# Kernel optimization log

Hardware: AMD Instinct MI355X
Metric: run time of the kernel (lower is better)

The kernel has to match this reference:

```python
import jax, jax.numpy as jnp
import numpy as np

N, E, H, NH, S, EF, K = 25000, 400000, 64, 4, 16, 8, 2
HS = H // NH  # head size


def _ln(x, w, b):
    m = x.mean(-1, keepdims=True)
    v = ((x - m) ** 2).mean(-1, keepdims=True)
    return (x - m) / jnp.sqrt(v + 1e-5) * w + b


def _seg_softmax(scores, seg, n):
    # scores: [E, NH], seg: [E] -> softmax over edges sharing the same dest node
    mx = jax.ops.segment_max(scores, seg, num_segments=n)
    e = jnp.exp(scores - mx[seg])
    s = jax.ops.segment_sum(e, seg, num_segments=n)
    return e / (s[seg] + 1e-9)


def _edge_layer(h, x_s, src, dest, ef, w1, w2, proj, gated):
    # h: [N,H] (already layer-normed). Gather, fused per-edge MLP (no bias).
    inp = jnp.concatenate([h[src], h[dest], x_s[src], x_s[dest], ef], axis=-1)  # [E,168]
    raw = jnp.maximum(inp @ w1.T, 0.0) @ w2.T  # [E,NH]
    if gated:
        w = jax.nn.sigmoid(raw)
    else:
        w = _seg_softmax(jax.nn.leaky_relu(raw) / jnp.sqrt(jnp.asarray(HS, raw.dtype)), dest, N)
    msg = h.reshape(N, NH, HS)[src] * w[:, :, None]          # [E,NH,HS]
    agg = jax.ops.segment_sum(msg, dest, num_segments=N)     # [N,NH,HS]
    return agg.reshape(N, H) @ proj.T, w


def _mlp(x, w1, b1, w2, b2):
    return jnp.maximum(x @ w1.T + b1, 0.0) @ w2.T + b2


def _forward(x, x_s, edge_features, fwd_w1, fwd_w2, fwd_proj, rev_w1, rev_w2, rev_proj,
             ln_w, ln_b, r_w1, r_b1, r_w2, r_b2, z_w1, z_b1, z_w2, z_b2,
             c_w1, c_b1, c_w2, c_b2, edge_index):
    src, dest = edge_index[0], edge_index[1]
    # forward-direction stacked attention hops
    h_fwd, fwd_ws = x, []
    for k in range(K):
        h_norm = _ln(h_fwd, ln_w, ln_b)
        msg, w = _edge_layer(h_norm, x_s, src, dest, edge_features,
                             fwd_w1[k], fwd_w2[k], fwd_proj[k], gated=False)
        h_fwd = h_fwd + msg
        fwd_ws.append(w)
    fwd_ws = jnp.stack(fwd_ws, axis=-1)  # [E,NH,K]
    # reverse-direction stacked gating hops (edge direction flipped)
    h_rev, rev_ws = x, []
    for k in range(K):
        h_norm = _ln(h_rev, ln_w, ln_b)
        msg, w = _edge_layer(h_norm, x_s, dest, src, edge_features,
                             rev_w1[k], rev_w2[k], rev_proj[k], gated=True)
        h_rev = h_rev + msg
        rev_ws.append(w)
    rev_ws = jnp.stack(rev_ws, axis=-1)  # [E,NH,K]
    messages = jnp.concatenate([h_fwd - x, h_rev - x], axis=-1)  # [N,2H]
    gate_input = jnp.concatenate([x, messages], axis=-1)          # [N,3H]
    r_gate = jax.nn.sigmoid(_mlp(gate_input, r_w1, r_b1, r_w2, r_b2))
    z_gate = jax.nn.sigmoid(_mlp(gate_input, z_w1, z_b1, z_w2, z_b2))
    cand_in = jnp.concatenate([r_gate * x, messages], axis=-1)
    cand = jnp.tanh(_mlp(cand_in, c_w1, c_b1, c_w2, c_b2))
    final_h = (1.0 - z_gate) * x + z_gate * cand
    return final_h, fwd_ws, rev_ws, z_gate, r_gate


def setup_inputs() -> dict:
    key = jax.random.key(0)
    ks = jax.random.split(key, 20)
    mlp_in = 2 * H + 2 * S + EF  # 168
    width = 2 * H                # 128
    gi, gw = 3 * H, 3 * H        # 192, 192

    def nrm(k, shape, fan_in):
        return jax.random.normal(k, shape, jnp.float32) / np.sqrt(fan_in)

    return {
        'x': jax.random.normal(ks[0], (N, H), jnp.float32),
        'x_s': jax.random.normal(ks[1], (N, S), jnp.float32),
        'edge_index': jax.random.randint(ks[2], (2, E), 0, N, jnp.int32),
        'edge_features': jax.random.normal(ks[3], (E, EF), jnp.float32),
        'fwd_w1': nrm(ks[4], (K, width, mlp_in), mlp_in),
        'fwd_w2': nrm(ks[5], (K, NH, width), width),
        'fwd_proj': nrm(ks[6], (K, H, H), H),
        'rev_w1': nrm(ks[7], (K, width, mlp_in), mlp_in),
        'rev_w2': nrm(ks[8], (K, NH, width), width),
        'rev_proj': nrm(ks[9], (K, H, H), H),
        'ln_w': jnp.ones((H,), jnp.float32),
        'ln_b': jnp.zeros((H,), jnp.float32),
        'r_w1': nrm(ks[10], (gw, gi), gi), 'r_b1': jnp.zeros((gw,), jnp.float32),
        'r_w2': nrm(ks[11], (H, gw), gw), 'r_b2': jnp.zeros((H,), jnp.float32),
        'z_w1': nrm(ks[12], (gw, gi), gi), 'z_b1': jnp.zeros((gw,), jnp.float32),
        'z_w2': nrm(ks[13], (H, gw), gw), 'z_b2': jnp.zeros((H,), jnp.float32),
        'c_w1': nrm(ks[14], (gw, gi), gi), 'c_b1': jnp.zeros((gw,), jnp.float32),
        'c_w2': nrm(ks[15], (H, gw), gw), 'c_b2': jnp.zeros((H,), jnp.float32),
    }


def reference(x, x_s, edge_index, edge_features, fwd_w1, fwd_w2, fwd_proj,
              rev_w1, rev_w2, rev_proj, ln_w, ln_b, r_w1, r_b1, r_w2, r_b2,
              z_w1, z_b1, z_w2, z_b2, c_w1, c_b1, c_w2, c_b2):
    return _forward(x, x_s, edge_features, fwd_w1, fwd_w2, fwd_proj,
                    rev_w1, rev_w2, rev_proj, ln_w, ln_b,
                    r_w1, r_b1, r_w2, r_b2, z_w1, z_b1, z_w2, z_b2,
                    c_w1, c_b1, c_w2, c_b2, edge_index)
```

## Files before the change

### kernel.cpp

```cpp
#include <hip/hip_runtime.h>
#include <math.h>

#define NN 25000
#define EE 400000
#define HH 64
#define NHEAD 4
#define SDIM 16
#define EFDIM 8
#define KHOP 2
#define MIN 168
#define WID 128
#define GIN 192
#define KP 96

typedef __attribute__((ext_vector_type(8))) short bf16x8;
typedef __attribute__((ext_vector_type(4))) float f32x4;
typedef unsigned short ushortT;
typedef unsigned int uintT;

__device__ __forceinline__ float wave_sum64(float v) {
#pragma unroll
  for (int m = 1; m <= 32; m <<= 1) v += __shfl_xor(v, m, 64);
  return v;
}

__device__ __forceinline__ ushortT f2b(float f) {
  uintT u = __float_as_uint(f);
  return (ushortT)((u + 0x7FFFu + ((u >> 16) & 1u)) >> 16);
}
__device__ __forceinline__ float b2f(ushortT h) {
  return __uint_as_float(((uintT)h) << 16);
}
__device__ __forceinline__ float b2f_lo(uintT u) { return __uint_as_float(u << 16); }
__device__ __forceinline__ float b2f_hi(uintT u) { return __uint_as_float(u & 0xffff0000u); }

__global__ void k_histo2(const int* __restrict__ src, const int* __restrict__ dst,
                         int* __restrict__ cnt_s, int* __restrict__ cnt_d) {
  int e = blockIdx.x * 256 + threadIdx.x;
  if (e < EE) {
    atomicAdd(&cnt_d[dst[e]], 1);
    atomicAdd(&cnt_s[src[e]], 1);
  }
}

__global__ void k_scan2(const int* __restrict__ cnt_d, const int* __restrict__ cnt_s,
                        int* __restrict__ rp_d, int* __restrict__ rp_s) {
  const int* cnt = blockIdx.x ? cnt_s : cnt_d;
  int* rp = blockIdx.x ? rp_s : rp_d;
  __shared__ int part[1024];
  int t = threadIdx.x;
  const int CH = (NN + 1023) / 1024;
  int base = t * CH;
  int s = 0;
  for (int i = 0; i < CH; ++i) {
    int j = base + i;
    if (j < NN) s += cnt[j];
  }
  part[t] = s;
  __syncthreads();
  for (int off = 1; off < 1024; off <<= 1) {
    int v = (t >= off) ? part[t - off] : 0;
    __syncthreads();
    part[t] += v;
    __syncthreads();
  }
  int run = (t == 0) ? 0 : part[t - 1];
  for (int i = 0; i < CH; ++i) {
    int j = base + i;
    if (j < NN) { rp[j] = run; run += cnt[j]; }
  }
  if (t == 1023) rp[NN] = run;
}

__global__ void k_scatter2(const int* __restrict__ src, const int* __restrict__ dst,
                           const int* __restrict__ rp_s, const int* __restrict__ rp_d,
                           int* __restrict__ cur_s, int* __restrict__ cur_d,
                           int* __restrict__ eid_s, int* __restrict__ eid_d) {
  int e = blockIdx.x * 256 + threadIdx.x;
  if (e < EE) {
    int nd = dst[e];
    int pd = atomicAdd(&cur_d[nd], 1);
    eid_d[rp_d[nd] + pd] = e;
    int ns = src[e];
    int ps = atomicAdd(&cur_s[ns], 1);
    eid_s[rp_s[ns] + ps] = e;
  }
}

__global__ __launch_bounds__(256) void k_sortseg2(const int* __restrict__ rp_d,
                                                  const int* __restrict__ rp_s,
                                                  int* __restrict__ eid_d,
                                                  int* __restrict__ eid_s) {
  int gw = blockIdx.x * 4 + (threadIdx.x >> 6);
  int lane = threadIdx.x & 63;
  if (gw >= 2 * NN) return;
  const int* rp = (gw < NN) ? rp_d : rp_s;
  int* eids = (gw < NN) ? eid_d : eid_s;
  int node = (gw < NN) ? gw : gw - NN;
  int beg = rp[node], end = rp[node + 1];
  int deg = end - beg;
  if (deg <= 1) return;
  if (deg <= 64) {
    int v = (lane < deg) ? eids[beg + lane] : 0x7fffffff;
#pragma unroll
    for (int k = 2; k <= 64; k <<= 1) {
#pragma unroll
      for (int j = k >> 1; j > 0; j >>= 1) {
        int other = __shfl_xor(v, j, 64);
        bool takeMin = (((lane & k) == 0) == ((lane & j) == 0));
        v = takeMin ? min(v, other) : max(v, other);
      }
    }
    if (lane < deg) eids[beg + lane] = v;
  } else if (lane == 0) {
    for (int i = beg + 1; i < end; ++i) {
      int v = eids[i];
      int j = i - 1;
      while (j >= beg && eids[j] > v) { eids[j + 1] = eids[j]; --j; }
      eids[j + 1] = v;
    }
  }
}

__global__ void k_mkpos2(const int* __restrict__ eid_d, const int* __restrict__ eid_s,
                         const int* __restrict__ src, const int* __restrict__ dst,
                         const float* __restrict__ ef, int4* __restrict__ pos_f,
                         int4* __restrict__ pos_r, float4* __restrict__ efs_f,
                         float4* __restrict__ efs_r) {
  int i = blockIdx.x * 256 + threadIdx.x;
  if (i >= EE) return;
  int e1 = eid_d[i];
  pos_f[i] = make_int4(e1, src[e1], dst[e1], 0);
  int e2 = eid_s[i];
  pos_r[i] = make_int4(e2, dst[e2], src[e2], 0);
  efs_f[2 * i] = *(const float4*)(ef + (size_t)e1 * EFDIM);
  efs_f[2 * i + 1] = *(const float4*)(ef + (size_t)e1 * EFDIM + 4);
  efs_r[2 * i] = *(const float4*)(ef + (size_t)e2 * EFDIM);
  efs_r[2 * i + 1] = *(const float4*)(ef + (size_t)e2 * EFDIM + 4);
}

#define PACKN (256 * KP + 8 * 128)
__global__ void k_pack_bf(const float* __restrict__ fw1, const float* __restrict__ rw1,
                          ushortT* __restrict__ pAB_all, float* __restrict__ pE_all) {
  int y = blockIdx.y;
  const float* w1 = (y < 2) ? fw1 + (size_t)y * WID * MIN
                            : rw1 + (size_t)(y - 2) * WID * MIN;
  ushortT* pAB = pAB_all + (size_t)y * 256 * KP;
  float* pE = pE_all + (size_t)y * 8 * 128;
  int i = blockIdx.x * 256 + threadIdx.x;
  if (i < 256 * KP) {
    int j = i / KP, k = i % KP;
    float v = 0.f;
    if (k < 80) {
      int row = (j < 128) ? j : j - 128;
      int col = (j < 128) ? (k < 64 ? k : k + 64) : (k < 64 ? k + 64 : k + 80);
      v = w1[row * MIN + col];
    }
    pAB[i] = f2b(v);
  } else if (i < PACKN) {
    int ii = i - 256 * KP;
    int f = ii >> 7, j = ii & 127;
    pE[ii] = w1[j * MIN + 160 + f];
  }
}

#define CW1 (GIN * GIN)
#define CW2 (HH * GIN)
__global__ void k_cvt6(const float* __restrict__ r_w1, const float* __restrict__ z_w1,
                       const float* __restrict__ c_w1, const float* __restrict__ r_w2,
                       const float* __restrict__ z_w2, const float* __restrict__ c_w2,
                       ushortT* __restrict__ rzw1, ushortT* __restrict__ cw1,
                       ushortT* __restrict__ rw2, ushortT* __restrict__ zw2,
                       ushortT* __restrict__ cw2) {
  int i = blockIdx.x * 256 + threadIdx.x;
  if (i < CW1) rzw1[i] = f2b(r_w1[i]);
  else if (i < 2 * CW1) rzw1[i] = f2b(z_w1[i - CW1]);
  else if (i < 3 * CW1) cw1[i - 2 * CW1] = f2b(c_w1[i - 2 * CW1]);
  else if (i < 3 * CW1 + CW2) rw2[i - 3 * CW1] = f2b(r_w2[i - 3 * CW1]);
  else if (i < 3 * CW1 + 2 * CW2) zw2[i - 3 * CW1 - CW2] = f2b(z_w2[i - 3 * CW1 - CW2]);
  else if (i < 3 * CW1 + 3 * CW2) cw2[i - 3 * CW1 - 2 * CW2] = f2b(c_w2[i - 3 * CW1 - 2 * CW2]);
}

__global__ __launch_bounds__(256) void k_ln2(const float* __restrict__ hf,
                                             const float* __restrict__ hr,
                                             const float* __restrict__ xs,
                                             const float* __restrict__ lw,
                                             const float* __restrict__ lb,
                                             ushortT* __restrict__ ncf,
                                             ushortT* __restrict__ ncr) {
  const float* h = blockIdx.y ? hr : hf;
  ushortT* nodecat = blockIdx.y ? ncr : ncf;
  int t = threadIdx.x;
  int node = blockIdx.x * 4 + (t >> 6), lane = t & 63;
  if (node >= NN) return;
  float v = h[(size_t)node * HH + lane];
  float mean = wave_sum64(v) * (1.0f / 64.0f);
  float d = v - mean;
  float var = wave_sum64(d * d) * (1.0f / 64.0f);
  nodecat[(size_t)node * KP + lane] = f2b(d * rsqrtf(var + 1e-5f) * lw[lane] + lb[lane]);
  if (lane < SDIM) {
    nodecat[(size_t)node * KP + HH + lane] = f2b(xs[(size_t)node * SDIM + lane]);
    nodecat[(size_t)node * KP + 80 + lane] = 0;
  }
}

__global__ __launch_bounds__(256) void k_proj2(
    const ushortT* __restrict__ Af, const ushortT* __restrict__ Ar,
    const ushortT* __restrict__ Wf, const ushortT* __restrict__ Wr,
    ushortT* __restrict__ Cf, ushortT* __restrict__ Cr) {
  const ushortT* A = blockIdx.y ? Ar : Af;
  const ushortT* W = blockIdx.y ? Wr : Wf;
  ushortT* C = blockIdx.y ? Cr : Cf;
  int w = threadIdx.x >> 6, l = threadIdx.x & 63;
  int m0 = blockIdx.x * 64 + w * 16;
  int rowa = m0 + (l & 15);
  int kb = l >> 4;
  bf16x8 afr0 = {0,0,0,0,0,0,0,0}, afr1 = afr0, afr2 = afr0;
  if (rowa < NN) {
    const ushortT* ap = A + (size_t)rowa * KP + kb * 8;
    afr0 = *(const bf16x8*)(ap);
    afr1 = *(const bf16x8*)(ap + 32);
    afr2 = *(const bf16x8*)(ap + 64);
  }
  int crow = m0 + (l >> 4) * 4;
  int ccol0 = l & 15;
  for (int n0 = 0; n0 < 256; n0 += 64) {
    f32x4 acc[4];
#pragma unroll
    for (int n = 0; n < 4; ++n) acc[n] = (f32x4){0.f, 0.f, 0.f, 0.f};
    const ushortT* wbase = W + (size_t)(n0 + (l & 15)) * KP + kb * 8;
#pragma unroll
    for (int n = 0; n < 4; ++n) {
      const ushortT* wp = wbase + (size_t)(16 * n) * KP;
      acc[n] = __builtin_amdgcn_mfma_f32_16x16x32_bf16(afr0, *(const bf16x8*)(wp), acc[n], 0, 0, 0);
      acc[n] = __builtin_amdgcn_mfma_f32_16x16x32_bf16(afr1, *(const bf16x8*)(wp + 32), acc[n], 0, 0, 0);
      acc[n] = __builtin_amdgcn_mfma_f32_16x16x32_bf16(afr2, *(const bf16x8*)(wp + 64), acc[n], 0, 0, 0);
    }
#pragma unroll
    for (int n = 0; n < 4; ++n) {
      int col = n0 + ccol0 + n * 16;
#pragma unroll
      for (int r = 0; r < 4; ++r) {
        int row = crow + r;
        if (row < NN) C[(size_t)row * 256 + col] = f2b(acc[n][r]);
      }
    }
  }
}

template <int ACT, int BF16OUT, int KD>
__global__ __launch_bounds__(256) void k_gemm2(
    const ushortT* __restrict__ A, int lda, const ushortT* __restrict__ W,
    const float* __restrict__ bias, void* __restrict__ Cout, int ldc, int M, int Nc,
    const float* __restrict__ zv, const float* __restrict__ xp) {
  constexpr int KS = KD / 32;
  int w = threadIdx.x >> 6, l = threadIdx.x & 63;
  int m0 = blockIdx.x * 64 + w * 16;
  int rowa = m0 + (l & 15);
  int kb = l >> 4;
  bf16x8 afr[KS];
#pragma unroll
  for (int ks = 0; ks < KS; ++ks) {
    afr[ks] = (bf16x8){0, 0, 0, 0, 0, 0, 0, 0};
    if (rowa < M) afr[ks] = *(const bf16x8*)(A + (size_t)rowa * lda + ks * 32 + kb * 8);
  }
  int crow = m0 + (l >> 4) * 4;
  int ccol0 = l & 15;
  for (int n0 = 0; n0 < Nc; n0 += 64) {
    f32x4 acc[4];
#pragma unroll
    for (int n = 0; n < 4; ++n) acc[n] = (f32x4){0.f, 0.f, 0.f, 0.f};
    const ushortT* wbase = W + (size_t)(n0 + (l & 15)) * KD + kb * 8;
#pragma unroll
    for (int n = 0; n < 4; ++n) {
      const ushortT* wp = wbase + (size_t)(16 * n) * KD;
#pragma unroll
      for (int ks = 0; ks < KS; ++ks)
        acc[n] = __builtin_amdgcn_mfma_f32_16x16x32_bf16(afr[ks], *(const bf16x8*)(wp + ks * 32),
                                                         acc[n], 0, 0, 0);
    }
#pragma unroll
    for (int n = 0; n < 4; ++n) {
      int col = n0 + ccol0 + n * 16;
      float bv = bias ? bias[col] : 0.f;
#pragma unroll
      for (int r = 0; r < 4; ++r) {
        int row = crow + r;
        if (row < M) {
          float v = acc[n][r] + bv;
          if (ACT == 1) v = fmaxf(v, 0.f);
          else if (ACT == 2) v = 1.f / (1.f + expf(-v));
          else if (ACT == 3) v = tanhf(v);
          else if (ACT == 5) {
            float z = zv[(size_t)row * HH + col];
            float xv = xp[(size_t)row * HH + col];
            v = (1.f - z) * xv + z * tanhf(v);
          }
          if (BF16OUT)
            ((ushortT*)Cout)[(size_t)row * ldc + col] = f2b(v);
          else
            ((float*)Cout)[(size_t)row * ldc + col] = v;
        }
      }
    }
  }
}

__global__ __launch_bounds__(256) void k_gemm_rz(
    const ushortT* __restrict__ hid, const ushortT* __restrict__ rw2,
    const ushortT* __restrict__ zw2, const float* __restrict__ rb2,
    const float* __restrict__ zb2, float* __restrict__ outR, float* __restrict__ outZ) {
  int y = blockIdx.y;
  const ushortT* A = hid + (y ? GIN : 0);
  const ushortT* W = y ? zw2 : rw2;
  const float* bias = y ? zb2 : rb2;
  float* C = y ? outZ : outR;
  constexpr int KS = GIN / 32;
  int w = threadIdx.x >> 6, l = threadIdx.x & 63;
  int m0 = blockIdx.x * 64 + w * 16;
  int rowa = m0 + (l & 15);
  int kb = l >> 4;
  bf16x8 afr[KS];
#pragma unroll
  for (int ks = 0; ks < KS; ++ks) {
    afr[ks] = (bf16x8){0, 0, 0, 0, 0, 0, 0, 0};
    if (rowa < NN) afr[ks] = *(const bf16x8*)(A + (size_t)rowa * 384 + ks * 32 + kb * 8);
  }
  int crow = m0 + (l >> 4) * 4;
  int ccol0 = l & 15;
  f32x4 acc[4];
#pragma unroll
  for (int n = 0; n < 4; ++n) acc[n] = (f32x4){0.f, 0.f, 0.f, 0.f};
  const ushortT* wbase = W + (size_t)(l & 15) * GIN + kb * 8;
#pragma unroll
  for (int n = 0; n < 4; ++n) {
    const ushortT* wp = wbase + (size_t)(16 * n) * GIN;
#pragma unroll
    for (int ks = 0; ks < KS; ++ks)
      acc[n] = __builtin_amdgcn_mfma_f32_16x16x32_bf16(afr[ks], *(const bf16x8*)(wp + ks * 32),
                                                       acc[n], 0, 0, 0);
  }
#pragma unroll
  for (int n = 0; n < 4; ++n) {
    int col = ccol0 + n * 16;
    float bv = bias[col];
#pragma unroll
    for (int r = 0; r < 4; ++r) {
      int row = crow + r;
      if (row < NN) {
        float v = acc[n][r] + bv;
        C[(size_t)row * HH + col] = 1.f / (1.f + expf(-v));
      }
    }
  }
}

__global__ __launch_bounds__(256) void k_edge3(
    const ushortT* __restrict__ cABf, const ushortT* __restrict__ cABr,
    const int4* __restrict__ pos_f, const int4* __restrict__ pos_r,
    const float4* __restrict__ efs_f, const float4* __restrict__ efs_r,
    const float* __restrict__ w1e_f, const float* __restrict__ w1e_r,
    const float* __restrict__ w2f, const float* __restrict__ w2r,
    float* __restrict__ s_seq, float* __restrict__ outRW,
    float* __restrict__ ws_seq, int hop) {
  int y = blockIdx.y;
  const ushortT* cAB = y ? cABr : cABf;
  const int4* pos = y ? pos_r : pos_f;
  const float4* efs = y ? efs_r : efs_f;
  const float* w1e = y ? w1e_r : w1e_f;
  const float* w2 = y ? w2r : w2f;
  __shared__ float w1e_s[8][128];
  __shared__ float w2_s[4][128];
  int t = threadIdx.x;
  for (int i = t; i < 1024; i += 256) w1e_s[i >> 7][i & 127] = w1e[i];
  for (int i = t; i < 512; i += 256) w2_s[i >> 7][i & 127] = w2[i];
  __syncthreads();
  int es = t >> 2, q = t & 3;
  size_t ii = (size_t)blockIdx.x * 64 + es;
  int4 pr = pos[ii];
  const ushortT* cA = cAB + (size_t)pr.y * 256;
  const ushortT* cBp = cAB + (size_t)pr.z * 256 + 128;
  float4 e0 = efs[2 * ii], e1 = efs[2 * ii + 1];
  float efv[8] = {e0.x, e0.y, e0.z, e0.w, e1.x, e1.y, e1.z, e1.w};
  float p[4] = {0.f, 0.f, 0.f, 0.f};
#pragma unroll
  for (int c = 0; c < 4; ++c) {
    int j = c * 32 + q * 8;
    uint4 ua4 = *(const uint4*)(cA + j);
    uint4 ub4 = *(const uint4*)(cBp + j);
    const uintT* au = (const uintT*)&ua4;
    const uintT* bu = (const uintT*)&ub4;
    float h[8];
#pragma unroll
    for (int i2 = 0; i2 < 4; ++i2) {
      h[2 * i2] = b2f_lo(au[i2]) + b2f_lo(bu[i2]);
      h[2 * i2 + 1] = b2f_hi(au[i2]) + b2f_hi(bu[i2]);
    }
#pragma unroll
    for (int f = 0; f < 8; ++f) {
      float ev = efv[f];
      float4 w0 = *(const float4*)(&w1e_s[f][j]);
      float4 w1v = *(const float4*)(&w1e_s[f][j + 4]);
      h[0] += ev * w0.x; h[1] += ev * w0.y; h[2] += ev * w0.z; h[3] += ev * w0.w;
      h[4] += ev * w1v.x; h[5] += ev * w1v.y; h[6] += ev * w1v.z; h[7] += ev * w1v.w;
    }
#pragma unroll
    for (int i2 = 0; i2 < 8; ++i2) h[i2] = fmaxf(h[i2], 0.f);
#pragma unroll
    for (int o = 0; o < 4; ++o) {
      float4 u0 = *(const float4*)(&w2_s[o][j]);
      float4 u1 = *(const float4*)(&w2_s[o][j + 4]);
      p[o] += h[0] * u0.x + h[1] * u0.y + h[2] * u0.z + h[3] * u0.w +
              h[4] * u1.x + h[5] * u1.y + h[6] * u1.z + h[7] * u1.w;
    }
  }
#pragma unroll
  for (int o = 0; o < 4; ++o) {
    p[o] += __shfl_xor(p[o], 1, 64);
    p[o] += __shfl_xor(p[o], 2, 64);
  }
  float pv = (q == 0) ? p[0] : (q == 1) ? p[1] : (q == 2) ? p[2] : p[3];
  if (y) {
    float sig = 1.f / (1.f + expf(-pv));
    outRW[(size_t)pr.x * (NHEAD * KHOP) + q * KHOP + hop] = sig;
    ws_seq[ii * 4 + q] = sig;
  } else {
    s_seq[ii * 4 + q] = (pv > 0.f ? pv : 0.01f * pv) * 0.25f;
  }
}

template <int SM>
__global__ __launch_bounds__(256) void k_softagg(
    const ushortT* __restrict__ hn_bf, const float* __restrict__ s_seq,
    const float* __restrict__ ws_seq, int hop, const int* __restrict__ rp,
    const int4* __restrict__ pos, const float* __restrict__ proj,
    float* __restrict__ h, float* __restrict__ wout) {
  __shared__ float proj_s[64][68];
  __shared__ float agg_s[4][64];
  __shared__ float w_s[4][64][4];
  int t = threadIdx.x;
  for (int i = t; i < 4096; i += 256) proj_s[i >> 6][i & 63] = proj[i];
  int wvi = t >> 6, lane = t & 63;
  int node = blockIdx.x * 4 + wvi;
  __syncthreads();

  float acc = 0.f;
  if (node < NN) {
    int beg = rp[node], end = rp[node + 1];
    int deg = end - beg;
    float mxv = 0.f, invv = 0.f;
    if (SM && deg > 0) {
      int li = lane >> 2, o = lane & 3;
      if (deg <= 64) {
        int i0 = beg + li;
        int ee4[4];
        float sv[4];
#pragma unroll
        for (int u = 0; u < 4; ++u) {
          int idx = i0 + u * 16;
          bool val = idx < end;
          int id2 = val ? idx : beg;
          ee4[u] = pos[id2].x;
          float v = s_seq[(size_t)id2 * 4 + o];
          sv[u] = val ? v : -1e30f;
        }
        float mx = fmaxf(fmaxf(sv[0], sv[1]), fmaxf(sv[2], sv[3]));
#pragma unroll
        for (int m = 4; m <= 32; m <<= 1) mx = fmaxf(mx, __shfl_xor(mx, m, 64));
        float ex[4];
        float sum = 0.f;
#pragma unroll
        for (int u = 0; u < 4; ++u) {
          ex[u] = (sv[u] > -1e29f) ? expf(sv[u] - mx) : 0.f;
          sum += ex[u];
        }
#pragma unroll
        for (int m = 4; m <= 32; m <<= 1) sum += __shfl_xor(sum, m, 64);
        float inv = 1.f / (sum + 1e-9f);
#pragma unroll
        for (int u = 0; u < 4; ++u) {
          if (i0 + u * 16 < end) {
            float wv = ex[u] * inv;
            wout[(size_t)ee4[u] * (NHEAD * KHOP) + o * KHOP + hop] = wv;
            w_s[wvi][li + u * 16][o] = wv;
          }
        }
      } else {
        float mx = -1e30f;
        for (int ii = beg + li; ii < end; ii += 16)
          mx = fmaxf(mx, s_seq[(size_t)ii * 4 + o]);
#pragma unroll
        for (int m = 4; m <= 32; m <<= 1) mx = fmaxf(mx, __shfl_xor(mx, m, 64));
        float sum = 0.f;
        for (int ii = beg + li; ii < end; ii += 16)
          sum += expf(s_seq[(size_t)ii * 4 + o] - mx);
#pragma unroll
        for (int m = 4; m <= 32; m <<= 1) sum += __shfl_xor(sum, m, 64);
        float inv = 1.f / (sum + 1e-9f);
        for (int ii = beg + li; ii < end; ii += 16) {
          wout[(size_t)pos[ii].x * (NHEAD * KHOP) + o * KHOP + hop] =
              expf(s_seq[(size_t)ii * 4 + o] - mx) * inv;
        }
        mxv = mx;
        invv = inv;
      }
    }
    int hd = lane >> 4;
    float mx_hd = 0.f, inv_hd = 0.f;
    if (SM) {
      mx_hd = __shfl(mxv, hd, 64);
      inv_hd = __shfl(invv, hd, 64);
    }
    bool useLds = (deg <= 64);
    for (int ii = beg; ii < end; ii += 8) {
      int idxv[8];
      int other[8];
      float wv8[8];
      float hv[8];
#pragma unroll
      for (int u = 0; u < 8; ++u) {
        int idx = ii + u;
        idxv[u] = (idx < end) ? idx : beg;
      }
#pragma unroll
      for (int u = 0; u < 8; ++u) other[u] = pos[idxv[u]].y;
#pragma unroll
      for (int u = 0; u < 8; ++u) {
        if (SM) {
          if (useLds)
            wv8[u] = w_s[wvi][idxv[u] - beg][hd];
          else
            wv8[u] = expf(s_seq[(size_t)idxv[u] * 4 + hd] - mx_hd) * inv_hd;
        } else {
          wv8[u] = ws_seq[(size_t)idxv[u] * 4 + hd];
        }
      }
#pragma unroll
      for (int u = 0; u < 8; ++u)
        hv[u] = b2f(hn_bf[(size_t)other[u] * KP + lane]);
#pragma unroll
      for (int u = 0; u < 8; ++u) {
        float w = (ii + u < end) ? wv8[u] : 0.f;
        acc += w * hv[u];
      }
    }
  }
  agg_s[wvi][lane] = acc;
  __syncthreads();
  if (node < NN) {
    float m = 0.f;
#pragma unroll
    for (int hh = 0; hh < 64; hh += 4) {
      float4 p = *(const float4*)(&proj_s[lane][hh]);
      m += p.x * agg_s[wvi][hh] + p.y * agg_s[wvi][hh + 1] +
           p.z * agg_s[wvi][hh + 2] + p.w * agg_s[wvi][hh + 3];
    }
    h[(size_t)node * HH + lane] += m;
  }
}

__global__ void k_gatein(const float* __restrict__ x, const float* __restrict__ hf,
                         const float* __restrict__ hr, ushortT* __restrict__ gi) {
  int g = blockIdx.x * 256 + threadIdx.x;
  if (g >= NN * HH) return;
  int node = g >> 6, j = g & 63;
  float xv = x[g];
  gi[(size_t)node * GIN + j] = f2b(xv);
  gi[(size_t)node * GIN + 64 + j] = f2b(hf[g] - xv);
  gi[(size_t)node * GIN + 128 + j] = f2b(hr[g] - xv);
}

__global__ void k_candin(const float* __restrict__ x, const float* __restrict__ r,
                         ushortT* __restrict__ gi) {
  int g = blockIdx.x * 256 + threadIdx.x;
  if (g >= NN * HH) return;
  gi[(size_t)(g >> 6) * GIN + (g & 63)] = f2b(r[g] * x[g]);
}

extern "C" void kernel_launch(void* const* d_in, const int* in_sizes, int n_in,
                              void* d_out, int out_size, void* d_ws, size_t ws_size,
                              hipStream_t stream) {
  const float* x = (const float*)d_in[0];
  const float* xs = (const float*)d_in[1];
  const int* ei = (const int*)d_in[2];
  const float* ef = (const float*)d_in[3];
  const float* fw1 = (const float*)d_in[4];
  const float* fw2 = (const float*)d_in[5];
  const float* fpj = (const float*)d_in[6];
  const float* rw1 = (const float*)d_in[7];
  const float* rw2 = (const float*)d_in[8];
  const float* rpj = (const float*)d_in[9];
  const float* lnw = (const float*)d_in[10];
  const float* lnb = (const float*)d_in[11];
  const float* r_w1 = (const float*)d_in[12];
  const float* r_b1 = (const float*)d_in[13];
  const float* r_w2 = (const float*)d_in[14];
  const float* r_b2 = (const float*)d_in[15];
  const float* z_w1 = (const float*)d_in[16];
  const float* z_b1 = (const float*)d_in[17];
  const float* z_w2 = (const float*)d_in[18];
  const float* z_b2 = (const float*)d_in[19];
  const float* c_w1 = (const float*)d_in[20];
  const float* c_b1 = (const float*)d_in[21];
  const float* c_w2 = (const float*)d_in[22];
  const float* c_b2 = (const float*)d_in[23];
  const int* srcp = ei;
  const int* dstp = ei + EE;

  float* outF = (float*)d_out;
  float* outFW = outF + (size_t)NN * HH;
  float* outRW = outFW + (size_t)EE * NHEAD * KHOP;
  float* outZ = outRW + (size_t)EE * NHEAD * KHOP;
  float* outR = outZ + (size_t)NN * HH;

  char* Wb = (char*)d_ws;
  size_t off = 0;
  auto alloc = [&](size_t bytes) -> void* {
    void* p = Wb + off;
    off += (bytes + 255) & ~(size_t)255;
    return p;
  };
  float* h_fwd = (float*)alloc((size_t)NN * HH * 4);
  float* h_rev = (float*)alloc((size_t)NN * HH * 4);
  ushortT* ncat_f = (ushortT*)alloc((size_t)NN * KP * 2);
  ushortT* ncat_r = (ushortT*)alloc((size_t)NN * KP * 2);
  float* s_seq = (float*)alloc((size_t)EE * NHEAD * 4);
  float* ws_seq = (float*)alloc((size_t)EE * NHEAD * 4);
  char* big = (char*)alloc((size_t)2 * NN * 256 * 2);
  ushortT* cAB_f = (ushortT*)big;
  ushortT* cAB_r = (ushortT*)(big + (size_t)NN * 256 * 2);
  ushortT* hid_bf = (ushortT*)big;
  ushortT* gi_bf = (ushortT*)alloc((size_t)NN * GIN * 2);
  ushortT* packAB_bf = (ushortT*)alloc((size_t)4 * 256 * KP * 2);
  float* packE = (float*)alloc((size_t)4 * 8 * 128 * 4);
  ushortT* rzw1_bf = (ushortT*)alloc((size_t)384 * GIN * 2);
  ushortT* rw2_bf = (ushortT*)alloc((size_t)HH * GIN * 2);
  ushortT* zw2_bf = (ushortT*)alloc((size_t)HH * GIN * 2);
  ushortT* cw1_bf = (ushortT*)alloc((size_t)GIN * GIN * 2);
  ushortT* cw2_bf = (ushortT*)alloc((size_t)HH * GIN * 2);
  float* rz_b1 = (float*)alloc(384 * 4);
  int* rp_d = (int*)alloc((NN + 8) * 4);
  int* rp_s = (int*)alloc((NN + 8) * 4);
  int* cur2 = (int*)alloc((size_t)2 * NN * 4);
  int* cur_d = cur2;
  int* cur_s = cur2 + NN;
  int* eid_d = (int*)alloc((size_t)EE * 4);
  int* eid_s = (int*)alloc((size_t)EE * 4);
  int4* pos_f = (int4*)alloc((size_t)EE * 16);
  int4* pos_r = (int4*)alloc((size_t)EE * 16);
  float4* efs_f = (float4*)alloc((size_t)EE * 32);
  float4* efs_r = (float4*)alloc((size_t)EE * 32);

  (void)hipMemcpyAsync(h_fwd, x, (size_t)NN * HH * 4, hipMemcpyDeviceToDevice, stream);
  (void)hipMemcpyAsync(h_rev, x, (size_t)NN * HH * 4, hipMemcpyDeviceToDevice, stream);
  (void)hipMemcpyAsync(rz_b1, r_b1, GIN * 4, hipMemcpyDeviceToDevice, stream);
  (void)hipMemcpyAsync(rz_b1 + GIN, z_b1, GIN * 4, hipMemcpyDeviceToDevice, stream);

  const int EB = (EE + 255) / 256, NW = (NN + 3) / 4;
  const int PB = (PACKN + 255) / 256;

  dim3 gPack(PB, 4);
  k_pack_bf<<<gPack, 256, 0, stream>>>(fw1, rw1, packAB_bf, packE);
  k_cvt6<<<(3 * CW1 + 3 * CW2 + 255) / 256, 256, 0, stream>>>(
      r_w1, z_w1, c_w1, r_w2, z_w2, c_w2, rzw1_bf, cw1_bf, rw2_bf, zw2_bf, cw2_bf);

  (void)hipMemsetAsync(cur2, 0, (size_t)2 * NN * 4, stream);
  k_histo2<<<EB, 256, 0, stream>>>(srcp, dstp, cur_s, cur_d);
  k_scan2<<<2, 1024, 0, stream>>>(cur_d, cur_s, rp_d, rp_s);
  (void)hipMemsetAsync(cur2, 0, (size_t)2 * NN * 4, stream);
  k_scatter2<<<EB, 256, 0, stream>>>(srcp, dstp, rp_s, rp_d, cur_s, cur_d, eid_s, eid_d);
  k_sortseg2<<<(2 * NN + 3) / 4, 256, 0, stream>>>(rp_d, rp_s, eid_d, eid_s);
  k_mkpos2<<<EB, 256, 0, stream>>>(eid_d, eid_s, srcp, dstp, ef, pos_f, pos_r, efs_f, efs_r);

  const int MB64 = (NN + 63) / 64;
  dim3 gLN(NW, 2), gProj(MB64, 2), gEdge(EE / 64, 2);
  for (int k = 0; k < KHOP; ++k) {
    k_ln2<<<gLN, 256, 0, stream>>>(h_fwd, h_rev, xs, lnw, lnb, ncat_f, ncat_r);
    k_proj2<<<gProj, 256, 0, stream>>>(ncat_f, ncat_r,
                                       packAB_bf + (size_t)k * 256 * KP,
                                       packAB_bf + (size_t)(2 + k) * 256 * KP,
                                       cAB_f, cAB_r);
    k_edge3<<<gEdge, 256, 0, stream>>>(cAB_f, cAB_r, pos_f, pos_r, efs_f, efs_r,
                                       packE + (size_t)k * 8 * 128,
                                       packE + (size_t)(2 + k) * 8 * 128,
                                       fw2 + (size_t)k * NHEAD * WID,
                                       rw2 + (size_t)k * NHEAD * WID,
                                       s_seq, outRW, ws_seq, k);
    k_softagg<1><<<NW, 256, 0, stream>>>(ncat_f, s_seq, nullptr, k, rp_d, pos_f,
                                         fpj + (size_t)k * HH * HH, h_fwd, outFW);
    k_softagg<0><<<NW, 256, 0, stream>>>(ncat_r, nullptr, ws_seq, k, rp_s, pos_r,
                                         rpj + (size_t)k * HH * HH, h_rev, nullptr);
  }

  k_gatein<<<(NN * HH) / 256, 256, 0, stream>>>(x, h_fwd, h_rev, gi_bf);
  k_gemm2<1, 1, GIN><<<MB64, 256, 0, stream>>>(gi_bf, GIN, rzw1_bf, rz_b1, hid_bf,
                                               384, NN, 384, nullptr, nullptr);
  dim3 gRZ(MB64, 2);
  k_gemm_rz<<<gRZ, 256, 0, stream>>>(hid_bf, rw2_bf, zw2_bf, r_b2, z_b2, outR, outZ);
  k_candin<<<(NN * HH) / 256, 256, 0, stream>>>(x, outR, gi_bf);
  k_gemm2<1, 1, GIN><<<MB64, 256, 0, stream>>>(gi_bf, GIN, cw1_bf, c_b1, hid_bf, GIN,
                                               NN, GIN, nullptr, nullptr);
  k_gemm2<5, 0, GIN><<<MB64, 256, 0, stream>>>(hid_bf, GIN, cw2_bf, c_b2, outF, HH,
                                               NN, HH, outZ, x);
}
```

Measured before the change: 609.5 us.

## Use fp16 packed math in edge MLP and fuse LN and gate prep into aggregation

The per-edge MLP now works in packed half2 arithmetic: the projected node features, edge features and second-layer weights are stored as fp16, halving gather bandwidth and doubling ALU throughput. LayerNorm for the next hop is fused into the aggregation kernel, and the forward and reverse aggregation launches are merged into one grid. Gate-input and candidate-input preparation are folded into the aggregation and r/z GEMM epilogues, removing separate kernels and extra passes over node arrays. The cost is reduced precision (fp16 range and accumulation inside the MLP) and more complex kernels.

```diff
diff --git a/kernel.cpp b/kernel.cpp
--- a/kernel.cpp
+++ b/kernel.cpp
@@ -1,4 +1,5 @@
 #include <hip/hip_runtime.h>
+#include <hip/hip_fp16.h>
 #include <math.h>
 
 #define NN 25000
@@ -31,8 +32,19 @@
 __device__ __forceinline__ float b2f(ushortT h) {
   return __uint_as_float(((uintT)h) << 16);
 }
-__device__ __forceinline__ float b2f_lo(uintT u) { return __uint_as_float(u << 16); }
-__device__ __forceinline__ float b2f_hi(uintT u) { return __uint_as_float(u & 0xffff0000u); }
+
+union U4H8 {
+  uint4 u;
+  __half2 h[4];
+};
+
+__device__ __forceinline__ __half2 relu2(__half2 v) {
+  union { __half2 h; uintT u; } x;
+  x.h = v;
+  uintT mask = ((x.u & 0x80008000u) >> 15) * 0xFFFFu;
+  x.u &= ~mask;
+  return x.h;
+}
 
 __global__ void k_histo2(const int* __restrict__ src, const int* __restrict__ dst,
                          int* __restrict__ cnt_s, int* __restrict__ cnt_d) {
@@ -125,28 +137,46 @@
 __global__ void k_mkpos2(const int* __restrict__ eid_d, const int* __restrict__ eid_s,
                          const int* __restrict__ src, const int* __restrict__ dst,
                          const float* __restrict__ ef, int4* __restrict__ pos_f,
-                         int4* __restrict__ pos_r, float4* __restrict__ efs_f,
-                         float4* __restrict__ efs_r) {
+                         int4* __restrict__ pos_r, uint4* __restrict__ efh_f,
+                         uint4* __restrict__ efh_r) {
   int i = blockIdx.x * 256 + threadIdx.x;
   if (i >= EE) return;
   int e1 = eid_d[i];
   pos_f[i] = make_int4(e1, src[e1], dst[e1], 0);
   int e2 = eid_s[i];
   pos_r[i] = make_int4(e2, dst[e2], src[e2], 0);
-  efs_f[2 * i] = *(const float4*)(ef + (size_t)e1 * EFDIM);
-  efs_f[2 * i + 1] = *(const float4*)(ef + (size_t)e1 * EFDIM + 4);
-  efs_r[2 * i] = *(const float4*)(ef + (size_t)e2 * EFDIM);
-  efs_r[2 * i + 1] = *(const float4*)(ef + (size_t)e2 * EFDIM + 4);
-}
-
-#define PACKN (256 * KP + 8 * 128)
+  {
+    float4 a0 = *(const float4*)(ef + (size_t)e1 * EFDIM);
+    float4 a1 = *(const float4*)(ef + (size_t)e1 * EFDIM + 4);
+    U4H8 u;
+    u.h[0] = __floats2half2_rn(a0.x, a0.y);
+    u.h[1] = __floats2half2_rn(a0.z, a0.w);
+    u.h[2] = __floats2half2_rn(a1.x, a1.y);
+    u.h[3] = __floats2half2_rn(a1.z, a1.w);
+    efh_f[i] = u.u;
+  }
+  {
+    float4 b0 = *(const float4*)(ef + (size_t)e2 * EFDIM);
+    float4 b1 = *(const float4*)(ef + (size_t)e2 * EFDIM + 4);
+    U4H8 u;
+    u.h[0] = __floats2half2_rn(b0.x, b0.y);
+    u.h[1] = __floats2half2_rn(b0.z, b0.w);
+    u.h[2] = __floats2half2_rn(b1.x, b1.y);
+    u.h[3] = __floats2half2_rn(b1.z, b1.w);
+    efh_r[i] = u.u;
+  }
+}
+
+#define PACKN (256 * KP + 512 + 256)
 __global__ void k_pack_bf(const float* __restrict__ fw1, const float* __restrict__ rw1,
-                          ushortT* __restrict__ pAB_all, float* __restrict__ pE_all) {
+                          const float* __restrict__ fw2, const float* __restrict__ rw2,
+                          ushortT* __restrict__ pAB_all, __half2* __restrict__ w1e2_all,
+                          __half2* __restrict__ w22_all) {
   int y = blockIdx.y;
   const float* w1 = (y < 2) ? fw1 + (size_t)y * WID * MIN
                             : rw1 + (size_t)(y - 2) * WID * MIN;
-  ushortT* pAB = pAB_all + (size_t)y * 256 * KP;
-  float* pE = pE_all + (size_t)y * 8 * 128;
+  const float* w2 = (y < 2) ? fw2 + (size_t)y * NHEAD * WID
+                            : rw2 + (size_t)(y - 2) * NHEAD * WID;
   int i = blockIdx.x * 256 + threadIdx.x;
   if (i < 256 * KP) {
     int j = i / KP, k = i % KP;
@@ -156,11 +186,16 @@
       int col = (j < 128) ? (k < 64 ? k : k + 64) : (k < 64 ? k + 64 : k + 80);
       v = w1[row * MIN + col];
     }
-    pAB[i] = f2b(v);
+    pAB_all[(size_t)y * 256 * KP + i] = f2b(v);
+  } else if (i < 256 * KP + 512) {
+    int jj = i - 256 * KP;
+    int f = jj >> 6, jp = jj & 63;
+    w1e2_all[y * 512 + jj] =
+        __floats2half2_rn(w1[(2 * jp) * MIN + 160 + f], w1[(2 * jp + 1) * MIN + 160 + f]);
   } else if (i < PACKN) {
-    int ii = i - 256 * KP;
-    int f = ii >> 7, j = ii & 127;
-    pE[ii] = w1[j * MIN + 160 + f];
+    int jj = i - 256 * KP - 512;
+    int o = jj >> 6, jp = jj & 63;
+    w22_all[y * 256 + jj] = __floats2half2_rn(w2[o * WID + 2 * jp], w2[o * WID + 2 * jp + 1]);
   }
 }
 
@@ -181,26 +216,31 @@
   else if (i < 3 * CW1 + 3 * CW2) cw2[i - 3 * CW1 - 2 * CW2] = f2b(c_w2[i - 3 * CW1 - 2 * CW2]);
 }
 
-__global__ __launch_bounds__(256) void k_ln2(const float* __restrict__ hf,
-                                             const float* __restrict__ hr,
-                                             const float* __restrict__ xs,
-                                             const float* __restrict__ lw,
-                                             const float* __restrict__ lb,
-                                             ushortT* __restrict__ ncf,
-                                             ushortT* __restrict__ ncr) {
-  const float* h = blockIdx.y ? hr : hf;
-  ushortT* nodecat = blockIdx.y ? ncr : ncf;
+__global__ __launch_bounds__(256) void k_ln_init(
+    const float* __restrict__ x, const float* __restrict__ xs,
+    const float* __restrict__ lw, const float* __restrict__ lb,
+    ushortT* __restrict__ ncf0, ushortT* __restrict__ ncr0,
+    ushortT* __restrict__ ncf1, ushortT* __restrict__ ncr1) {
   int t = threadIdx.x;
   int node = blockIdx.x * 4 + (t >> 6), lane = t & 63;
   if (node >= NN) return;
-  float v = h[(size_t)node * HH + lane];
+  float v = x[(size_t)node * HH + lane];
   float mean = wave_sum64(v) * (1.0f / 64.0f);
   float d = v - mean;
   float var = wave_sum64(d * d) * (1.0f / 64.0f);
-  nodecat[(size_t)node * KP + lane] = f2b(d * rsqrtf(var + 1e-5f) * lw[lane] + lb[lane]);
+  ushortT val = f2b(d * rsqrtf(var + 1e-5f) * lw[lane] + lb[lane]);
+  ncf0[(size_t)node * KP + lane] = val;
+  ncr0[(size_t)node * KP + lane] = val;
   if (lane < SDIM) {
-    nodecat[(size_t)node * KP + HH + lane] = f2b(xs[(size_t)node * SDIM + lane]);
-    nodecat[(size_t)node * KP + 80 + lane] = 0;
+    ushortT xv = f2b(xs[(size_t)node * SDIM + lane]);
+    ncf0[(size_t)node * KP + HH + lane] = xv;
+    ncr0[(size_t)node * KP + HH + lane] = xv;
+    ncf1[(size_t)node * KP + HH + lane] = xv;
+    ncr1[(size_t)node * KP + HH + lane] = xv;
+    ncf0[(size_t)node * KP + 80 + lane] = 0;
+    ncr0[(size_t)node * KP + 80 + lane] = 0;
+    ncf1[(size_t)node * KP + 80 + lane] = 0;
+    ncr1[(size_t)node * KP + 80 + lane] = 0;
   }
 }
 
@@ -242,7 +282,8 @@
 #pragma unroll
       for (int r = 0; r < 4; ++r) {
         int row = crow + r;
-        if (row < NN) C[(size_t)row * 256 + col] = f2b(acc[n][r]);
+        if (row < NN)
+          C[(size_t)row * 256 + col] = __half_as_ushort(__float2half(acc[n][r]));
       }
     }
   }
@@ -309,7 +350,8 @@
 __global__ __launch_bounds__(256) void k_gemm_rz(
     const ushortT* __restrict__ hid, const ushortT* __restrict__ rw2,
     const ushortT* __restrict__ zw2, const float* __restrict__ rb2,
-    const float* __restrict__ zb2, float* __restrict__ outR, float* __restrict__ outZ) {
+    const float* __restrict__ zb2, float* __restrict__ outR, float* __restrict__ outZ,
+    const float* __restrict__ x, ushortT* __restrict__ gi) {
   int y = blockIdx.y;
   const ushortT* A = hid + (y ? GIN : 0);
   const ushortT* W = y ? zw2 : rw2;
@@ -349,7 +391,10 @@
       int row = crow + r;
       if (row < NN) {
         float v = acc[n][r] + bv;
-        C[(size_t)row * HH + col] = 1.f / (1.f + expf(-v));
+        float sig = 1.f / (1.f + expf(-v));
+        C[(size_t)row * HH + col] = sig;
+        if (y == 0)
+          gi[(size_t)row * GIN + col] = f2b(sig * x[(size_t)row * HH + col]);
       }
     }
   }
@@ -358,68 +403,74 @@
 __global__ __launch_bounds__(256) void k_edge3(
     const ushortT* __restrict__ cABf, const ushortT* __restrict__ cABr,
     const int4* __restrict__ pos_f, const int4* __restrict__ pos_r,
-    const float4* __restrict__ efs_f, const float4* __restrict__ efs_r,
-    const float* __restrict__ w1e_f, const float* __restrict__ w1e_r,
-    const float* __restrict__ w2f, const float* __restrict__ w2r,
+    const uint4* __restrict__ efh_f, const uint4* __restrict__ efh_r,
+    const __half2* __restrict__ w1e2_f, const __half2* __restrict__ w1e2_r,
+    const __half2* __restrict__ w22_f, const __half2* __restrict__ w22_r,
     float* __restrict__ s_seq, float* __restrict__ outRW,
     float* __restrict__ ws_seq, int hop) {
   int y = blockIdx.y;
-  const ushortT* cAB = y ? cABr : cABf;
+  const __half2* cAB2 = (const __half2*)(y ? cABr : cABf);
   const int4* pos = y ? pos_r : pos_f;
-  const float4* efs = y ? efs_r : efs_f;
-  const float* w1e = y ? w1e_r : w1e_f;
-  const float* w2 = y ? w2r : w2f;
-  __shared__ float w1e_s[8][128];
-  __shared__ float w2_s[4][128];
+  const uint4* efh = y ? efh_r : efh_f;
+  const __half2* w1e2 = y ? w1e2_r : w1e2_f;
+  const __half2* w22 = y ? w22_r : w22_f;
+  __shared__ __half2 w1e2_s[8][64];
+  __shared__ __half2 w22_s[4][64];
   int t = threadIdx.x;
-  for (int i = t; i < 1024; i += 256) w1e_s[i >> 7][i & 127] = w1e[i];
-  for (int i = t; i < 512; i += 256) w2_s[i >> 7][i & 127] = w2[i];
+  for (int i = t; i < 512; i += 256) w1e2_s[i >> 6][i & 63] = w1e2[i];
+  if (t < 256) w22_s[t >> 6][t & 63] = w22[t];
   __syncthreads();
   int es = t >> 2, q = t & 3;
   size_t ii = (size_t)blockIdx.x * 64 + es;
   int4 pr = pos[ii];
-  const ushortT* cA = cAB + (size_t)pr.y * 256;
-  const ushortT* cBp = cAB + (size_t)pr.z * 256 + 128;
-  float4 e0 = efs[2 * ii], e1 = efs[2 * ii + 1];
-  float efv[8] = {e0.x, e0.y, e0.z, e0.w, e1.x, e1.y, e1.z, e1.w};
-  float p[4] = {0.f, 0.f, 0.f, 0.f};
+  const __half2* cA2 = cAB2 + (size_t)pr.y * 128;
+  const __half2* cB2 = cAB2 + (size_t)pr.z * 128 + 64;
+  U4H8 efu;
+  efu.u = efh[ii];
+  __half2 efb[8];
+#pragma unroll
+  for (int f2v = 0; f2v < 4; ++f2v) {
+    efb[2 * f2v] = __half2half2(__low2half(efu.h[f2v]));
+    efb[2 * f2v + 1] = __half2half2(__high2half(efu.h[f2v]));
+  }
+  float pf[4] = {0.f, 0.f, 0.f, 0.f};
 #pragma unroll
   for (int c = 0; c < 4; ++c) {
-    int j = c * 32 + q * 8;
-    uint4 ua4 = *(const uint4*)(cA + j);
-    uint4 ub4 = *(const uint4*)(cBp + j);
-    const uintT* au = (const uintT*)&ua4;
-    const uintT* bu = (const uintT*)&ub4;
-    float h[8];
-#pragma unroll
-    for (int i2 = 0; i2 < 4; ++i2) {
-      h[2 * i2] = b2f_lo(au[i2]) + b2f_lo(bu[i2]);
-      h[2 * i2 + 1] = b2f_hi(au[i2]) + b2f_hi(bu[i2]);
-    }
+    int jp0 = c * 16 + q * 4;
+    U4H8 ua, ub;
+    ua.u = *(const uint4*)(cA2 + jp0);
+    ub.u = *(const uint4*)(cB2 + jp0);
+    __half2 h2v[4];
+#pragma unroll
+    for (int i2 = 0; i2 < 4; ++i2) h2v[i2] = __hadd2(ua.h[i2], ub.h[i2]);
 #pragma unroll
     for (int f = 0; f < 8; ++f) {
-      float ev = efv[f];
-      float4 w0 = *(const float4*)(&w1e_s[f][j]);
-      float4 w1v = *(const float4*)(&w1e_s[f][j + 4]);
-      h[0] += ev * w0.x; h[1] += ev * w0.y; h[2] += ev * w0.z; h[3] += ev * w0.w;
-      h[4] += ev * w1v.x; h[5] += ev * w1v.y; h[6] += ev * w1v.z; h[7] += ev * w1v.w;
-    }
-#pragma unroll
-    for (int i2 = 0; i2 < 8; ++i2) h[i2] = fmaxf(h[i2], 0.f);
+      U4H8 wv;
+      wv.u = *(const uint4*)(&w1e2_s[f][jp0]);
+#pragma unroll
+      for (int i2 = 0; i2 < 4; ++i2) h2v[i2] = __hfma2(efb[f], wv.h[i2], h2v[i2]);
+    }
+#pragma unroll
+    for (int i2 = 0; i2 < 4; ++i2) h2v[i2] = relu2(h2v[i2]);
 #pragma unroll
     for (int o = 0; o < 4; ++o) {
-      float4 u0 = *(const float4*)(&w2_s[o][j]);
-      float4 u1 = *(const float4*)(&w2_s[o][j + 4]);
-      p[o] += h[0] * u0.x + h[1] * u0.y + h[2] * u0.z + h[3] * u0.w +
-              h[4] * u1.x + h[5] * u1.y + h[6] * u1.z + h[7] * u1.w;
-    }
-  }
-#pragma unroll
-  for (int o = 0; o < 4; ++o) {
-    p[o] += __shfl_xor(p[o], 1, 64);
-    p[o] += __shfl_xor(p[o], 2, 64);
-  }
-  float pv = (q == 0) ? p[0] : (q == 1) ? p[1] : (q == 2) ? p[2] : p[3];
+      U4H8 wv;
+      wv.u = *(const uint4*)(&w22_s[o][jp0]);
+      __half2 p2 = __hmul2(h2v[0], wv.h[0]);
+      p2 = __hfma2(h2v[1], wv.h[1], p2);
+      p2 = __hfma2(h2v[2], wv.h[2], p2);
+      p2 = __hfma2(h2v[3], wv.h[3], p2);
+      pf[o] += __low2float(p2) + __high2float(p2);
+    }
+  }
+#pragma unroll
+  for (int m = 1; m <= 2; m <<= 1) {
+    pf[0] += __shfl_xor(pf[0], m, 64);
+    pf[1] += __shfl_xor(pf[1], m, 64);
+    pf[2] += __shfl_xor(pf[2], m, 64);
+    pf[3] += __shfl_xor(pf[3], m, 64);
+  }
+  float pv = (q == 0) ? pf[0] : (q == 1) ? pf[1] : (q == 2) ? pf[2] : pf[3];
   if (y) {
     float sig = 1.f / (1.f + expf(-pv));
     outRW[(size_t)pr.x * (NHEAD * KHOP) + q * KHOP + hop] = sig;
@@ -429,12 +480,23 @@
   }
 }
 
-template <int SM>
-__global__ __launch_bounds__(256) void k_softagg(
-    const ushortT* __restrict__ hn_bf, const float* __restrict__ s_seq,
-    const float* __restrict__ ws_seq, int hop, const int* __restrict__ rp,
-    const int4* __restrict__ pos, const float* __restrict__ proj,
-    float* __restrict__ h, float* __restrict__ wout) {
+template <int DO_LN, int DO_GATE>
+__global__ __launch_bounds__(256) void k_softagg3(
+    const ushortT* __restrict__ ncf, const ushortT* __restrict__ ncr,
+    ushortT* __restrict__ ncf_n, ushortT* __restrict__ ncr_n,
+    const float* __restrict__ s_seq, const float* __restrict__ ws_seq, int hop,
+    const int* __restrict__ rp_d, const int* __restrict__ rp_s,
+    const int4* __restrict__ pos_f, const int4* __restrict__ pos_r,
+    const float* __restrict__ proj_f, const float* __restrict__ proj_r,
+    float* __restrict__ h_f, float* __restrict__ h_r, float* __restrict__ wout,
+    const float* __restrict__ lnw, const float* __restrict__ lnb,
+    const float* __restrict__ x, ushortT* __restrict__ gi) {
+  int y = blockIdx.y;
+  const ushortT* hn_bf = y ? ncr : ncf;
+  const int* rp = y ? rp_s : rp_d;
+  const int4* pos = y ? pos_r : pos_f;
+  const float* proj = y ? proj_r : proj_f;
+  float* h = y ? h_r : h_f;
   __shared__ float proj_s[64][68];
   __shared__ float agg_s[4][64];
   __shared__ float w_s[4][64][4];
@@ -445,11 +507,13 @@
   __syncthreads();
 
   float acc = 0.f;
+  int beg = 0, end = 0;
   if (node < NN) {
-    int beg = rp[node], end = rp[node + 1];
+    beg = rp[node];
+    end = rp[node + 1];
     int deg = end - beg;
     float mxv = 0.f, invv = 0.f;
-    if (SM && deg > 0) {
+    if (y == 0 && deg > 0) {
       int li = lane >> 2, o = lane & 3;
       if (deg <= 64) {
         int i0 = beg + li;
@@ -507,11 +571,11 @@
     }
     int hd = lane >> 4;
     float mx_hd = 0.f, inv_hd = 0.f;
-    if (SM) {
+    if (y == 0) {
       mx_hd = __shfl(mxv, hd, 64);
       inv_hd = __shfl(invv, hd, 64);
     }
-    bool useLds = (deg <= 64);
+    bool useLds = ((end - beg) <= 64);
     for (int ii = beg; ii < end; ii += 8) {
       int idxv[8];
       int other[8];
@@ -526,7 +590,7 @@
       for (int u = 0; u < 8; ++u) other[u] = pos[idxv[u]].y;
 #pragma unroll
       for (int u = 0; u < 8; ++u) {
-        if (SM) {
+        if (y == 0) {
           if (useLds)
             wv8[u] = w_s[wvi][idxv[u] - beg][hd];
           else
@@ -555,26 +619,26 @@
       m += p.x * agg_s[wvi][hh] + p.y * agg_s[wvi][hh + 1] +
            p.z * agg_s[wvi][hh + 2] + p.w * agg_s[wvi][hh + 3];
     }
-    h[(size_t)node * HH + lane] += m;
-  }
-}
-
-__global__ void k_gatein(const float* __restrict__ x, const float* __restrict__ hf,
-                         const float* __restrict__ hr, ushortT* __restrict__ gi) {
-  int g = blockIdx.x * 256 + threadIdx.x;
-  if (g >= NN * HH) return;
-  int node = g >> 6, j = g & 63;
-  float xv = x[g];
-  gi[(size_t)node * GIN + j] = f2b(xv);
-  gi[(size_t)node * GIN + 64 + j] = f2b(hf[g] - xv);
-  gi[(size_t)node * GIN + 128 + j] = f2b(hr[g] - xv);
-}
-
-__global__ void k_candin(const float* __restrict__ x, const float* __restrict__ r,
-                         ushortT* __restrict__ gi) {
-  int g = blockIdx.x * 256 + threadIdx.x;
-  if (g >= NN * HH) return;
-  gi[(size_t)(g >> 6) * GIN + (g & 63)] = f2b(r[g] * x[g]);
+    size_t g = (size_t)node * HH + lane;
+    float hnew = h[g] + m;
+    h[g] = hnew;
+    if (DO_LN) {
+      float mean = wave_sum64(hnew) * (1.0f / 64.0f);
+      float d = hnew - mean;
+      float var = wave_sum64(d * d) * (1.0f / 64.0f);
+      ushortT val = f2b(d * rsqrtf(var + 1e-5f) * lnw[lane] + lnb[lane]);
+      (y ? ncr_n : ncf_n)[(size_t)node * KP + lane] = val;
+    }
+    if (DO_GATE) {
+      float xv = x[g];
+      if (y == 0) {
+        gi[(size_t)node * GIN + lane] = f2b(xv);
+        gi[(size_t)node * GIN + 64 + lane] = f2b(hnew - xv);
+      } else {
+        gi[(size_t)node * GIN + 128 + lane] = f2b(hnew - xv);
+      }
+    }
+  }
 }
 
 extern "C" void kernel_launch(void* const* d_in, const int* in_sizes, int n_in,
@@ -622,8 +686,10 @@
   };
   float* h_fwd = (float*)alloc((size_t)NN * HH * 4);
   float* h_rev = (float*)alloc((size_t)NN * HH * 4);
-  ushortT* ncat_f = (ushortT*)alloc((size_t)NN * KP * 2);
-  ushortT* ncat_r = (ushortT*)alloc((size_t)NN * KP * 2);
+  ushortT* ncat_f0 = (ushortT*)alloc((size_t)NN * KP * 2);
+  ushortT* ncat_r0 = (ushortT*)alloc((size_t)NN * KP * 2);
+  ushortT* ncat_f1 = (ushortT*)alloc((size_t)NN * KP * 2);
+  ushortT* ncat_r1 = (ushortT*)alloc((size_t)NN * KP * 2);
   float* s_seq = (float*)alloc((size_t)EE * NHEAD * 4);
   float* ws_seq = (float*)alloc((size_t)EE * NHEAD * 4);
   char* big = (char*)alloc((size_t)2 * NN * 256 * 2);
@@ -632,7 +698,8 @@
   ushortT* hid_bf = (ushortT*)big;
   ushortT* gi_bf = (ushortT*)alloc((size_t)NN * GIN * 2);
   ushortT* packAB_bf = (ushortT*)alloc((size_t)4 * 256 * KP * 2);
-  float* packE = (float*)alloc((size_t)4 * 8 * 128 * 4);
+  __half2* w1e2h = (__half2*)alloc((size_t)4 * 512 * 4);
+  __half2* w22h = (__half2*)alloc((size_t)4 * 256 * 4);
   ushortT* rzw1_bf = (ushortT*)alloc((size_t)384 * GIN * 2);
   ushortT* rw2_bf = (ushortT*)alloc((size_t)HH * GIN * 2);
   ushortT* zw2_bf = (ushortT*)alloc((size_t)HH * GIN * 2);
@@ -648,8 +715,8 @@
   int* eid_s = (int*)alloc((size_t)EE * 4);
   int4* pos_f = (int4*)alloc((size_t)EE * 16);
   int4* pos_r = (int4*)alloc((size_t)EE * 16);
-  float4* efs_f = (float4*)alloc((size_t)EE * 32);
-  float4* efs_r = (float4*)alloc((size_t)EE * 32);
+  uint4* efh_f = (uint4*)alloc((size_t)EE * 16);
+  uint4* efh_r = (uint4*)alloc((size_t)EE * 16);
 
   (void)hipMemcpyAsync(h_fwd, x, (size_t)NN * HH * 4, hipMemcpyDeviceToDevice, stream);
   (void)hipMemcpyAsync(h_rev, x, (size_t)NN * HH * 4, hipMemcpyDeviceToDevice, stream);
@@ -660,7 +727,7 @@
   const int PB = (PACKN + 255) / 256;
 
   dim3 gPack(PB, 4);
-  k_pack_bf<<<gPack, 256, 0, stream>>>(fw1, rw1, packAB_bf, packE);
+  k_pack_bf<<<gPack, 256, 0, stream>>>(fw1, rw1, fw2, rw2, packAB_bf, w1e2h, w22h);
   k_cvt6<<<(3 * CW1 + 3 * CW2 + 255) / 256, 256, 0, stream>>>(
       r_w1, z_w1, c_w1, r_w2, z_w2, c_w2, rzw1_bf, cw1_bf, rw2_bf, zw2_bf, cw2_bf);
 
@@ -670,34 +737,42 @@
   (void)hipMemsetAsync(cur2, 0, (size_t)2 * NN * 4, stream);
   k_scatter2<<<EB, 256, 0, stream>>>(srcp, dstp, rp_s, rp_d, cur_s, cur_d, eid_s, eid_d);
   k_sortseg2<<<(2 * NN + 3) / 4, 256, 0, stream>>>(rp_d, rp_s, eid_d, eid_s);
-  k_mkpos2<<<EB, 256, 0, stream>>>(eid_d, eid_s, srcp, dstp, ef, pos_f, pos_r, efs_f, efs_r);
+  k_mkpos2<<<EB, 256, 0, stream>>>(eid_d, eid_s, srcp, dstp, ef, pos_f, pos_r, efh_f, efh_r);
+
+  k_ln_init<<<NW, 256, 0, stream>>>(x, xs, lnw, lnb, ncat_f0, ncat_r0, ncat_f1, ncat_r1);
 
   const int MB64 = (NN + 63) / 64;
-  dim3 gLN(NW, 2), gProj(MB64, 2), gEdge(EE / 64, 2);
+  dim3 gProj(MB64, 2), gEdge(EE / 64, 2), gAgg(NW, 2);
   for (int k = 0; k < KHOP; ++k) {
-    k_ln2<<<gLN, 256, 0, stream>>>(h_fwd, h_rev, xs, lnw, lnb, ncat_f, ncat_r);
-    k_proj2<<<gProj, 256, 0, stream>>>(ncat_f, ncat_r,
+    const ushortT* nf = k ? ncat_f1 : ncat_f0;
+    const ushortT* nr = k ? ncat_r1 : ncat_r0;
+    k_proj2<<<gProj, 256, 0, stream>>>(nf, nr,
                                        packAB_bf + (size_t)k * 256 * KP,
                                        packAB_bf + (size_t)(2 + k) * 256 * KP,
                                        cAB_f, cAB_r);
-    k_edge3<<<gEdge, 256, 0, stream>>>(cAB_f, cAB_r, pos_f, pos_r, efs_f, efs_r,
-                                       packE + (size_t)k * 8 * 128,
-                                       packE + (size_t)(2 + k) * 8 * 128,
-                                       fw2 + (size_t)k * NHEAD * WID,
-                                       rw2 + (size_t)k * NHEAD * WID,
+    k_edge3<<<gEdge, 256, 0, stream>>>(cAB_f, cAB_r, pos_f, pos_r, efh_f, efh_r,
+                                       w1e2h + (size_t)k * 512,
+                                       w1e2h + (size_t)(2 + k) * 512,
+                                       w22h + (size_t)k * 256,
+                                       w22h + (size_t)(2 + k) * 256,
                                        s_seq, outRW, ws_seq, k);
-    k_softagg<1><<<NW, 256, 0, stream>>>(ncat_f, s_seq, nullptr, k, rp_d, pos_f,
-                                         fpj + (size_t)k * HH * HH, h_fwd, outFW);
-    k_softagg<0><<<NW, 256, 0, stream>>>(ncat_r, nullptr, ws_seq, k, rp_s, pos_r,
-                                         rpj + (size_t)k * HH * HH, h_rev, nullptr);
-  }
-
-  k_gatein<<<(NN * HH) / 256, 256, 0, stream>>>(x, h_fwd, h_rev, gi_bf);
+    if (k == 0)
+      k_softagg3<1, 0><<<gAgg, 256, 0, stream>>>(
+          nf, nr, ncat_f1, ncat_r1, s_seq, ws_seq, k, rp_d, rp_s, pos_f, pos_r,
+          fpj + (size_t)k * HH * HH, rpj + (size_t)k * HH * HH, h_fwd, h_rev, outFW,
+          lnw, lnb, x, gi_bf);
+    else
+      k_softagg3<0, 1><<<gAgg, 256, 0, stream>>>(
+          nf, nr, ncat_f1, ncat_r1, s_seq, ws_seq, k, rp_d, rp_s, pos_f, pos_r,
+          fpj + (size_t)k * HH * HH, rpj + (size_t)k * HH * HH, h_fwd, h_rev, outFW,
+          lnw, lnb, x, gi_bf);
+  }
+
   k_gemm2<1, 1, GIN><<<MB64, 256, 0, stream>>>(gi_bf, GIN, rzw1_bf, rz_b1, hid_bf,
                                                384, NN, 384, nullptr, nullptr);
   dim3 gRZ(MB64, 2);
-  k_gemm_rz<<<gRZ, 256, 0, stream>>>(hid_bf, rw2_bf, zw2_bf, r_b2, z_b2, outR, outZ);
-  k_candin<<<(NN * HH) / 256, 256, 0, stream>>>(x, outR, gi_bf);
+  k_gemm_rz<<<gRZ, 256, 0, stream>>>(hid_bf, rw2_bf, zw2_bf, r_b2, z_b2, outR, outZ,
+                                     x, gi_bf);
   k_gemm2<1, 1, GIN><<<MB64, 256, 0, stream>>>(gi_bf, GIN, cw1_bf, c_b1, hid_bf, GIN,
                                                NN, GIN, nullptr, nullptr);
   k_gemm2<5, 0, GIN><<<MB64, 256, 0, stream>>>(hid_bf, GIN, cw2_bf, c_b2, outF, HH,
```

Measured after the change: 547.0 us. -10.2%, faster.
